# Kernel tuning notes

Measured on AMD Instinct MI355X. Metric: run time of the kernel, lower is better.

## Reference

```python
import jax, jax.numpy as jnp
import numpy as np

GROUPS = 32
EPS = 1e-5

def group_norm(x, w, b):
    # x: [B, C, T]
    B, C, T = x.shape
    g = x.reshape(B, GROUPS, C // GROUPS, T)
    mu = g.mean(axis=(2, 3), keepdims=True)
    var = g.var(axis=(2, 3), keepdims=True)
    g = (g - mu) * jax.lax.rsqrt(var + EPS)
    return g.reshape(B, C, T) * w[None, :, None] + b[None, :, None]

def conv1x1(x, w, b):
    # x: [B, C, T], w: [O, C], b: [O]
    return jnp.einsum('oc,bct->bot', w, x) + b[None, :, None]

def setup_inputs() -> dict:
    key = jax.random.key(0)
    ks = jax.random.split(key, 10)
    B, C, H, W = 128, 512, 16, 16
    d = {}
    d['criminal_cond'] = jax.random.normal(ks[0], (B, C, H, W), jnp.float32)
    d['morph_cond'] = jax.random.normal(ks[1], (B, C, H, W), jnp.float32)
    d['norm_w'] = jax.random.uniform(ks[2], (C,), jnp.float32, 0.5, 1.5)
    d['norm_b'] = 0.02 * jax.random.normal(ks[3], (C,), jnp.float32)
    d['qkv_w'] = jax.random.normal(ks[4], (3 * C, C), jnp.float32) / np.sqrt(C)
    d['qkv_b'] = 0.02 * jax.random.normal(ks[5], (3 * C,), jnp.float32)
    d['ekv_w'] = jax.random.normal(ks[6], (2 * C, C), jnp.float32) / np.sqrt(C)
    d['ekv_b'] = 0.02 * jax.random.normal(ks[7], (2 * C,), jnp.float32)
    d['proj_w'] = jax.random.normal(ks[8], (C, C), jnp.float32) / np.sqrt(C)
    d['proj_b'] = 0.02 * jax.random.normal(ks[9], (C,), jnp.float32)
    return d

def reference(criminal_cond, morph_cond, norm_w, norm_b, qkv_w, qkv_b, ekv_w, ekv_b, proj_w, proj_b):
    B, C, H, W = criminal_cond.shape
    x = criminal_cond.reshape(B, C, H * W)          # [B, C, T]
    cond = morph_cond.reshape(B, C, H * W)          # [B, C, S], S == T here
    h = group_norm(x, norm_w, norm_b)
    qkv = conv1x1(h, qkv_w, qkv_b)                  # [B, 3C, T]
    q, k, v = jnp.split(qkv, 3, axis=1)
    ekv = conv1x1(cond, ekv_w, ekv_b)               # [B, 2C, S]
    ek, ev = jnp.split(ekv, 2, axis=1)
    k = jnp.concatenate([ek, k], axis=-1)           # [B, C, S+T]
    v = jnp.concatenate([ev, v], axis=-1)
    scale = 1.0 / np.sqrt(np.sqrt(C))               # single head, head_dim = C
    logits = jnp.einsum('bct,bcs->bts', q * scale, k * scale)
    w = jax.nn.softmax(logits, axis=-1)             # [B, T, S+T]
    a = jnp.einsum('bts,bcs->bct', w, v)            # [B, C, T]
    hout = conv1x1(a, proj_w, proj_b)
    attn_out = (x + hout).reshape(B, C, H, W)
    return 2.0 * morph_cond - attn_out
```

## Files before the change

### kernel.cpp

```cpp
#include <hip/hip_runtime.h>
#include <hip/hip_bf16.h>
#include <math.h>

#define NB 128
#define NC 512
#define NT 256
#define NL 512
#define NG 32
#define SCALE2 0.04419417382415922f

typedef __attribute__((ext_vector_type(8))) short bf16x8;
typedef __attribute__((ext_vector_type(4))) float f32x4;
typedef __attribute__((ext_vector_type(4))) unsigned short u16x4;
typedef __attribute__((ext_vector_type(8))) unsigned short u16x8;
typedef __hip_bfloat16 bf16;

struct Params {
  const float *x, *morph, *qkvb, *ekvb, *projb;
  const bf16 *wq, *we, *wp;
  bf16 *hT, *mT, *qT, *kfT, *vf;
  float *out;
  int b0;
};

enum { M_QKV = 0, M_EKV = 1 };

__device__ inline unsigned short f2bf_bits(float f) {
  bf16 h = __float2bfloat16(f);
  return *reinterpret_cast<unsigned short*>(&h);
}

__device__ inline void gld16(const void* g, void* lds) {
  __builtin_amdgcn_global_load_lds(
      (const __attribute__((address_space(1))) unsigned int*)g,
      (__attribute__((address_space(3))) unsigned int*)lds, 16, 0, 0);
}

__global__ __launch_bounds__(256) void gn_stats_k(const float* __restrict__ x,
                                                  float* __restrict__ stats) {
  const int bg = blockIdx.x;
  const float4* p4 = (const float4*)(x + (size_t)bg * 4096);
  float s = 0.f, s2 = 0.f;
  #pragma unroll
  for (int i = 0; i < 4; ++i) {
    float4 v = p4[threadIdx.x + i * 256];
    s  += v.x + v.y + v.z + v.w;
    s2 += v.x * v.x + v.y * v.y + v.z * v.z + v.w * v.w;
  }
  #pragma unroll
  for (int off = 32; off; off >>= 1) {
    s  += __shfl_down(s, off);
    s2 += __shfl_down(s2, off);
  }
  __shared__ float red[8];
  const int wave = threadIdx.x >> 6, lane = threadIdx.x & 63;
  if (lane == 0) { red[wave * 2] = s; red[wave * 2 + 1] = s2; }
  __syncthreads();
  if (threadIdx.x == 0) {
    float S = 0.f, S2 = 0.f;
    for (int w = 0; w < 4; ++w) { S += red[w * 2]; S2 += red[w * 2 + 1]; }
    float mu = S * (1.0f / 4096.0f);
    float var = S2 * (1.0f / 4096.0f) - mu * mu;
    stats[bg * 2]     = mu;
    stats[bg * 2 + 1] = rsqrtf(var + 1e-5f);
  }
}

__global__ __launch_bounds__(256) void cvt_k(const float* __restrict__ s,
                                             bf16* __restrict__ d, int n) {
  int i = blockIdx.x * 256 + threadIdx.x;
  if (i < n) d[i] = __float2bfloat16(s[i]);
}

__global__ __launch_bounds__(256) void transpose2_k(const float* __restrict__ x,
                                                    const float* __restrict__ morph,
                                                    bf16* __restrict__ hT,
                                                    bf16* __restrict__ mT,
                                                    const float* __restrict__ stats,
                                                    const float* __restrict__ gnw,
                                                    const float* __restrict__ gnb,
                                                    int b0, int nbc) {
  __shared__ float sm[64][65];
  const int z = blockIdx.z;
  const int norm = (z < nbc) ? 1 : 0;
  const int lb = norm ? z : z - nbc;
  const int gb = b0 + lb;
  const float* src = norm ? x : morph;
  bf16* dst = norm ? hT : mT;
  const int t0 = blockIdx.x * 64, c0 = blockIdx.y * 64;
  const int tx = threadIdx.x & 15, ty = threadIdx.x >> 4;
  #pragma unroll
  for (int ci = 0; ci < 4; ++ci) {
    const int c = ty + ci * 16;
    const int cg = c0 + c;
    float4 v = *(const float4*)&src[((size_t)gb * NC + cg) * NT + t0 + tx * 4];
    if (norm) {
      float mu = stats[(gb * NG + (cg >> 4)) * 2];
      float rs = stats[(gb * NG + (cg >> 4)) * 2 + 1];
      float wv = gnw[cg], bv = gnb[cg];
      v.x = (v.x - mu) * rs * wv + bv;
      v.y = (v.y - mu) * rs * wv + bv;
      v.z = (v.z - mu) * rs * wv + bv;
      v.w = (v.w - mu) * rs * wv + bv;
    }
    sm[c][tx * 4 + 0] = v.x; sm[c][tx * 4 + 1] = v.y;
    sm[c][tx * 4 + 2] = v.z; sm[c][tx * 4 + 3] = v.w;
  }
  __syncthreads();
  const int t = threadIdx.x >> 2, cq = threadIdx.x & 3;
  u16x8 pk0, pk1;
  #pragma unroll
  for (int k = 0; k < 8; ++k) pk0[k] = f2bf_bits(sm[cq * 16 + k][t]);
  #pragma unroll
  for (int k = 0; k < 8; ++k) pk1[k] = f2bf_bits(sm[cq * 16 + 8 + k][t]);
  bf16* d = dst + ((size_t)lb * NT + t0 + t) * NC + c0 + cq * 16;
  *(u16x8*)d = pk0;
  *(u16x8*)(d + 8) = pk1;
}

template <int MODE>
__global__ __launch_bounds__(256) void gemm_k(Params P) {
  __shared__ unsigned short As[128][32];
  __shared__ unsigned short Bs[128][32];
  const int lb = blockIdx.x;
  const int m0 = blockIdx.y * 128;
  const int n0 = blockIdx.z * 128;
  const int tid = threadIdx.x;
  const int lane = tid & 63, w = tid >> 6;
  const int wr = w >> 1, wc = w & 1;
  const int ln = lane & 15, kq = lane >> 4;

  const bf16 *Ab, *Bb;
  if (MODE == M_QKV) { Ab = P.hT + (size_t)lb * NT * NC; Bb = P.wq; }
  else               { Ab = P.mT + (size_t)lb * NT * NC; Bb = P.we; }

  const char* Abase = (const char*)(Ab + (size_t)m0 * 512);
  const char* Bbase = (const char*)(Bb + (size_t)n0 * 512);

  const int r_lo = w * 32 + (lane >> 2);
  const int cid16 = (lane & 3) * 16;

  f32x4 acc[4][4] = {};

  for (int k0 = 0; k0 < 512; k0 += 32) {
    const size_t kb = (size_t)k0 * 2 + cid16;
    #pragma unroll
    for (int h = 0; h < 2; ++h) {
      const int rw = r_lo + h * 16;
      gld16(Abase + (size_t)rw * 1024 + kb, (char*)As + w * 2048 + h * 1024);
      gld16(Bbase + (size_t)rw * 1024 + kb, (char*)Bs + w * 2048 + h * 1024);
    }
    __syncthreads();
    bf16x8 af[4], bfr[4];
    #pragma unroll
    for (int i = 0; i < 4; ++i)
      af[i] = *(const bf16x8*)&As[wr * 64 + i * 16 + ln][kq * 8];
    #pragma unroll
    for (int j = 0; j < 4; ++j)
      bfr[j] = *(const bf16x8*)&Bs[wc * 64 + j * 16 + ln][kq * 8];
    #pragma unroll
    for (int i = 0; i < 4; ++i)
      #pragma unroll
      for (int j = 0; j < 4; ++j)
        acc[i][j] = __builtin_amdgcn_mfma_f32_16x16x32_bf16(af[i], bfr[j], acc[i][j], 0, 0, 0);
    __syncthreads();
  }

  #pragma unroll
  for (int i = 0; i < 4; ++i) {
    const int ig = m0 + wr * 64 + i * 16 + kq * 4;
    #pragma unroll
    for (int j = 0; j < 4; ++j) {
      const int jg = n0 + wc * 64 + j * 16 + ln;
      f32x4 a = acc[i][j];
      if (MODE == M_QKV) {
        float bias = P.qkvb[jg];
        if (jg < 512) {
          bf16* d = P.qT + ((size_t)lb * NT + ig) * NC + jg;
          #pragma unroll
          for (int r = 0; r < 4; ++r) d[(size_t)r * NC] = __float2bfloat16(a[r] + bias);
        } else if (jg < 1024) {
          bf16* d = P.kfT + ((size_t)lb * NL + 256 + ig) * NC + (jg - 512);
          #pragma unroll
          for (int r = 0; r < 4; ++r) d[(size_t)r * NC] = __float2bfloat16(a[r] + bias);
        } else {
          u16x4 pk;
          #pragma unroll
          for (int r = 0; r < 4; ++r) pk[r] = f2bf_bits(a[r] + bias);
          *(u16x4*)(P.vf + ((size_t)lb * NC + (jg - 1024)) * NL + 256 + ig) = pk;
        }
      } else {
        float bias = P.ekvb[jg];
        if (jg < 512) {
          bf16* d = P.kfT + ((size_t)lb * NL + ig) * NC + jg;
          #pragma unroll
          for (int r = 0; r < 4; ++r) d[(size_t)r * NC] = __float2bfloat16(a[r] + bias);
        } else {
          u16x4 pk;
          #pragma unroll
          for (int r = 0; r < 4; ++r) pk[r] = f2bf_bits(a[r] + bias);
          *(u16x4*)(P.vf + ((size_t)lb * NC + (jg - 512)) * NL + ig) = pk;
        }
      }
    }
  }
}

__global__ __launch_bounds__(256) void attn_k(Params P) {
  __shared__ unsigned short Abuf[32][32];
  __shared__ unsigned short Bbuf[512][32];
  __shared__ unsigned short Pbuf[32][520];
  __shared__ float redm[4][32];
  __shared__ float reds[4][32];

  const int lb = blockIdx.x, gb = P.b0 + lb;
  const int t0 = blockIdx.y * 32;
  const int tid = threadIdx.x;
  const int lane = tid & 63, w = tid >> 6;
  const int ln = lane & 15, kq = lane >> 4;
  const int srow = lane >> 2;
  const int scol = (lane & 3) * 16;

  const char* qg  = (const char*)(P.qT  + ((size_t)lb * NT + t0) * NC);
  const char* kg  = (const char*)(P.kfT + (size_t)lb * NL * NC);
  const char* vg  = (const char*)(P.vf  + (size_t)lb * NC * NL);
  const char* wpg = (const char*)P.wp;

  f32x4 sa[2][8] = {};
  bf16x8 af[2], bfr[8];

  for (int k0 = 0; k0 < 512; k0 += 32) {
    const size_t koff = (size_t)k0 * 2 + scol;
    if (w < 2)
      gld16(qg + (size_t)(w * 16 + srow) * 1024 + koff, (char*)Abuf + w * 1024);
    #pragma unroll
    for (int h = 0; h < 8; ++h)
      gld16(kg + (size_t)(w * 128 + h * 16 + srow) * 1024 + koff,
            (char*)Bbuf + w * 8192 + h * 1024);
    __syncthreads();
    af[0] = *(const bf16x8*)&Abuf[ln][kq * 8];
    af[1] = *(const bf16x8*)&Abuf[16 + ln][kq * 8];
    #pragma unroll
    for (int j = 0; j < 8; ++j)
      bfr[j] = *(const bf16x8*)&Bbuf[w * 128 + j * 16 + ln][kq * 8];
    #pragma unroll
    for (int i = 0; i < 2; ++i)
      #pragma unroll
      for (int j = 0; j < 8; ++j)
        sa[i][j] = __builtin_amdgcn_mfma_f32_16x16x32_bf16(af[i], bfr[j], sa[i][j], 0, 0, 0);
    __syncthreads();
  }

  float mx[2][4], sum[2][4], inv[2][4];
  #pragma unroll
  for (int i = 0; i < 2; ++i)
    #pragma unroll
    for (int r = 0; r < 4; ++r) {
      float m = -1e30f;
      #pragma unroll
      for (int j = 0; j < 8; ++j) m = fmaxf(m, sa[i][j][r]);
      mx[i][r] = m;
    }
  #pragma unroll
  for (int off = 1; off < 16; off <<= 1)
    #pragma unroll
    for (int i = 0; i < 2; ++i)
      #pragma unroll
      for (int r = 0; r < 4; ++r) mx[i][r] = fmaxf(mx[i][r], __shfl_xor(mx[i][r], off));
  if (ln == 0)
    #pragma unroll
    for (int i = 0; i < 2; ++i)
      #pragma unroll
      for (int r = 0; r < 4; ++r) redm[w][i * 16 + kq * 4 + r] = mx[i][r];
  __syncthreads();
  #pragma unroll
  for (int i = 0; i < 2; ++i)
    #pragma unroll
    for (int r = 0; r < 4; ++r) {
      const int row = i * 16 + kq * 4 + r;
      mx[i][r] = fmaxf(fmaxf(redm[0][row], redm[1][row]),
                       fmaxf(redm[2][row], redm[3][row]));
      sum[i][r] = 0.f;
    }
  #pragma unroll
  for (int i = 0; i < 2; ++i)
    #pragma unroll
    for (int j = 0; j < 8; ++j)
      #pragma unroll
      for (int r = 0; r < 4; ++r) {
        float e = __expf(SCALE2 * (sa[i][j][r] - mx[i][r]));
        sa[i][j][r] = e;
        sum[i][r] += e;
      }
  #pragma unroll
  for (int off = 1; off < 16; off <<= 1)
    #pragma unroll
    for (int i = 0; i < 2; ++i)
      #pragma unroll
      for (int r = 0; r < 4; ++r) sum[i][r] += __shfl_xor(sum[i][r], off);
  if (ln == 0)
    #pragma unroll
    for (int i = 0; i < 2; ++i)
      #pragma unroll
      for (int r = 0; r < 4; ++r) reds[w][i * 16 + kq * 4 + r] = sum[i][r];
  __syncthreads();
  #pragma unroll
  for (int i = 0; i < 2; ++i)
    #pragma unroll
    for (int r = 0; r < 4; ++r) {
      const int row = i * 16 + kq * 4 + r;
      inv[i][r] = 1.0f / (reds[0][row] + reds[1][row] + reds[2][row] + reds[3][row]);
    }
  #pragma unroll
  for (int i = 0; i < 2; ++i)
    #pragma unroll
    for (int j = 0; j < 8; ++j)
      #pragma unroll
      for (int r = 0; r < 4; ++r)
        Pbuf[i * 16 + kq * 4 + r][w * 128 + j * 16 + ln] = f2bf_bits(sa[i][j][r] * inv[i][r]);
  __syncthreads();

  f32x4 oa[2][8] = {};
  for (int k0 = 0; k0 < 512; k0 += 32) {
    const size_t koff = (size_t)k0 * 2 + scol;
    #pragma unroll
    for (int h = 0; h < 8; ++h)
      gld16(vg + (size_t)(w * 128 + h * 16 + srow) * 1024 + koff,
            (char*)Bbuf + w * 8192 + h * 1024);
    __syncthreads();
    af[0] = *(const bf16x8*)&Pbuf[ln][k0 + kq * 8];
    af[1] = *(const bf16x8*)&Pbuf[16 + ln][k0 + kq * 8];
    #pragma unroll
    for (int j = 0; j < 8; ++j)
      bfr[j] = *(const bf16x8*)&Bbuf[w * 128 + j * 16 + ln][kq * 8];
    #pragma unroll
    for (int i = 0; i < 2; ++i)
      #pragma unroll
      for (int j = 0; j < 8; ++j)
        oa[i][j] = __builtin_amdgcn_mfma_f32_16x16x32_bf16(af[i], bfr[j], oa[i][j], 0, 0, 0);
    __syncthreads();
  }

  #pragma unroll
  for (int i = 0; i < 2; ++i)
    #pragma unroll
    for (int j = 0; j < 8; ++j)
      #pragma unroll
      for (int r = 0; r < 4; ++r)
        Pbuf[i * 16 + kq * 4 + r][w * 128 + j * 16 + ln] = f2bf_bits(oa[i][j][r]);
  __syncthreads();

  f32x4 za[2][8] = {};
  for (int k0 = 0; k0 < 512; k0 += 32) {
    const size_t koff = (size_t)k0 * 2 + scol;
    #pragma unroll
    for (int h = 0; h < 8; ++h)
      gld16(wpg + (size_t)(w * 128 + h * 16 + srow) * 1024 + koff,
            (char*)Bbuf + w * 8192 + h * 1024);
    __syncthreads();
    af[0] = *(const bf16x8*)&Pbuf[ln][k0 + kq * 8];
    af[1] = *(const bf16x8*)&Pbuf[16 + ln][k0 + kq * 8];
    #pragma unroll
    for (int j = 0; j < 8; ++j)
      bfr[j] = *(const bf16x8*)&Bbuf[w * 128 + j * 16 + ln][kq * 8];
    #pragma unroll
    for (int i = 0; i < 2; ++i)
      #pragma unroll
      for (int j = 0; j < 8; ++j)
        za[i][j] = __builtin_amdgcn_mfma_f32_16x16x32_bf16(af[i], bfr[j], za[i][j], 0, 0, 0);
    __syncthreads();
  }

  #pragma unroll
  for (int i = 0; i < 2; ++i) {
    const int trow = t0 + i * 16 + kq * 4;
    #pragma unroll
    for (int j = 0; j < 8; ++j) {
      const int c = w * 128 + j * 16 + ln;
      const float bias = P.projb[c];
      const size_t idx = ((size_t)gb * NC + c) * NT + trow;
      float4 mo = *(const float4*)&P.morph[idx];
      float4 xx = *(const float4*)&P.x[idx];
      f32x4 o;
      o[0] = 2.0f * mo.x - xx.x - (za[i][j][0] + bias);
      o[1] = 2.0f * mo.y - xx.y - (za[i][j][1] + bias);
      o[2] = 2.0f * mo.z - xx.z - (za[i][j][2] + bias);
      o[3] = 2.0f * mo.w - xx.w - (za[i][j][3] + bias);
      *(f32x4*)&P.out[idx] = o;
    }
  }
}

extern "C" void kernel_launch(void* const* d_in, const int* in_sizes, int n_in,
                              void* d_out, int out_size, void* d_ws, size_t ws_size,
                              hipStream_t stream) {
  const float* x     = (const float*)d_in[0];
  const float* morph = (const float*)d_in[1];
  const float* gnw   = (const float*)d_in[2];
  const float* gnb   = (const float*)d_in[3];
  const float* qkvw  = (const float*)d_in[4];
  const float* qkvb  = (const float*)d_in[5];
  const float* ekvw  = (const float*)d_in[6];
  const float* ekvb  = (const float*)d_in[7];
  const float* projw = (const float*)d_in[8];
  const float* projb = (const float*)d_in[9];

  bf16* wq = (bf16*)d_ws;
  bf16* we = wq + 786432;
  bf16* wp = we + 524288;
  float* stats = (float*)(wp + 262144);
  bf16* pb = (bf16*)(stats + 8192);

  const size_t per_b = 917504;
  const size_t fixed = (size_t)(786432 + 524288 + 262144) * 2 + 8192 * 4;
  int nbc = NB;
  while (nbc > 1 && fixed + (size_t)nbc * per_b * 2 > ws_size) nbc >>= 1;

  Params P;
  P.x = x; P.morph = morph; P.qkvb = qkvb; P.ekvb = ekvb; P.projb = projb;
  P.wq = wq; P.we = we; P.wp = wp;
  P.hT  = pb;  pb += (size_t)nbc * 131072;
  P.mT  = pb;  pb += (size_t)nbc * 131072;
  P.qT  = pb;  pb += (size_t)nbc * 131072;
  P.kfT = pb;  pb += (size_t)nbc * 262144;
  P.vf  = pb;
  P.out = (float*)d_out;

  gn_stats_k<<<dim3(NB * NG), dim3(256), 0, stream>>>(x, stats);
  cvt_k<<<dim3(3072), dim3(256), 0, stream>>>(qkvw, wq, 786432);
  cvt_k<<<dim3(2048), dim3(256), 0, stream>>>(ekvw, we, 524288);
  cvt_k<<<dim3(1024), dim3(256), 0, stream>>>(projw, wp, 262144);

  for (int b0 = 0; b0 < NB; b0 += nbc) {
    P.b0 = b0;
    transpose2_k<<<dim3(4, 8, 2 * nbc), dim3(256), 0, stream>>>(
        x, morph, P.hT, P.mT, stats, gnw, gnb, b0, nbc);
    gemm_k<M_QKV><<<dim3(nbc, 2, 12), dim3(256), 0, stream>>>(P);
    gemm_k<M_EKV><<<dim3(nbc, 2, 8),  dim3(256), 0, stream>>>(P);
    attn_k       <<<dim3(nbc, 8),     dim3(256), 0, stream>>>(P);
  }
}
```

Baseline: 539.2 us.

## Load attention MFMA operands directly from global memory, dropping LDS staging

The three GEMM phases in the attention kernel (QK^T, PV, output projection) now read their B operands, and for QK^T also the A operand, straight from global memory into registers. The shared-memory staging buffers and the per-iteration barriers are removed. This cuts LDS traffic and synchronisation and frees shared memory for occupancy. In exchange, each wave issues strided 16-byte global loads with no cross-wave reuse, relying on the L1/L2 caches for the K/V/Wp tiles that every block rereads.

```diff
diff --git a/kernel.cpp b/kernel.cpp
--- a/kernel.cpp
+++ b/kernel.cpp
@@ -207,8 +207,6 @@
 }
 
 __global__ __launch_bounds__(256) void attn_k(Params P) {
-  __shared__ unsigned short Abuf[32][32];
-  __shared__ unsigned short Bbuf[512][32];
   __shared__ unsigned short Pbuf[32][520];
   __shared__ float redm[4][32];
   __shared__ float reds[4][32];
@@ -218,37 +216,30 @@
   const int tid = threadIdx.x;
   const int lane = tid & 63, w = tid >> 6;
   const int ln = lane & 15, kq = lane >> 4;
-  const int srow = lane >> 2;
-  const int scol = (lane & 3) * 16;
-
-  const char* qg  = (const char*)(P.qT  + ((size_t)lb * NT + t0) * NC);
-  const char* kg  = (const char*)(P.kfT + (size_t)lb * NL * NC);
-  const char* vg  = (const char*)(P.vf  + (size_t)lb * NC * NL);
-  const char* wpg = (const char*)P.wp;
+
+  const bf16* qg  = P.qT  + ((size_t)lb * NT + t0) * NC;
+  const bf16* kg  = P.kfT + (size_t)lb * NL * NC;
+  const bf16* vg  = P.vf  + (size_t)lb * NC * NL;
+  const bf16* wpg = P.wp;
 
   f32x4 sa[2][8] = {};
   bf16x8 af[2], bfr[8];
 
-  for (int k0 = 0; k0 < 512; k0 += 32) {
-    const size_t koff = (size_t)k0 * 2 + scol;
-    if (w < 2)
-      gld16(qg + (size_t)(w * 16 + srow) * 1024 + koff, (char*)Abuf + w * 1024);
-    #pragma unroll
-    for (int h = 0; h < 8; ++h)
-      gld16(kg + (size_t)(w * 128 + h * 16 + srow) * 1024 + koff,
-            (char*)Bbuf + w * 8192 + h * 1024);
-    __syncthreads();
-    af[0] = *(const bf16x8*)&Abuf[ln][kq * 8];
-    af[1] = *(const bf16x8*)&Abuf[16 + ln][kq * 8];
-    #pragma unroll
-    for (int j = 0; j < 8; ++j)
-      bfr[j] = *(const bf16x8*)&Bbuf[w * 128 + j * 16 + ln][kq * 8];
-    #pragma unroll
-    for (int i = 0; i < 2; ++i)
+  {
+    const bf16* qa0 = qg + (size_t)ln * NC + kq * 8;
+    const bf16* kb0 = kg + (size_t)(w * 128 + ln) * NC + kq * 8;
+    for (int k0 = 0; k0 < 512; k0 += 32) {
+      af[0] = *(const bf16x8*)(qa0 + k0);
+      af[1] = *(const bf16x8*)(qa0 + (size_t)16 * NC + k0);
       #pragma unroll
       for (int j = 0; j < 8; ++j)
-        sa[i][j] = __builtin_amdgcn_mfma_f32_16x16x32_bf16(af[i], bfr[j], sa[i][j], 0, 0, 0);
-    __syncthreads();
+        bfr[j] = *(const bf16x8*)(kb0 + (size_t)j * 16 * NC + k0);
+      #pragma unroll
+      for (int i = 0; i < 2; ++i)
+        #pragma unroll
+        for (int j = 0; j < 8; ++j)
+          sa[i][j] = __builtin_amdgcn_mfma_f32_16x16x32_bf16(af[i], bfr[j], sa[i][j], 0, 0, 0);
+    }
   }
 
   float mx[2][4], sum[2][4], inv[2][4];
@@ -321,25 +312,22 @@
   __syncthreads();
 
   f32x4 oa[2][8] = {};
-  for (int k0 = 0; k0 < 512; k0 += 32) {
-    const size_t koff = (size_t)k0 * 2 + scol;
-    #pragma unroll
-    for (int h = 0; h < 8; ++h)
-      gld16(vg + (size_t)(w * 128 + h * 16 + srow) * 1024 + koff,
-            (char*)Bbuf + w * 8192 + h * 1024);
-    __syncthreads();
-    af[0] = *(const bf16x8*)&Pbuf[ln][k0 + kq * 8];
-    af[1] = *(const bf16x8*)&Pbuf[16 + ln][k0 + kq * 8];
-    #pragma unroll
-    for (int j = 0; j < 8; ++j)
-      bfr[j] = *(const bf16x8*)&Bbuf[w * 128 + j * 16 + ln][kq * 8];
-    #pragma unroll
-    for (int i = 0; i < 2; ++i)
+  {
+    const bf16* vb0 = vg + (size_t)(w * 128 + ln) * NL + kq * 8;
+    for (int k0 = 0; k0 < 512; k0 += 32) {
+      af[0] = *(const bf16x8*)&Pbuf[ln][k0 + kq * 8];
+      af[1] = *(const bf16x8*)&Pbuf[16 + ln][k0 + kq * 8];
       #pragma unroll
       for (int j = 0; j < 8; ++j)
-        oa[i][j] = __builtin_amdgcn_mfma_f32_16x16x32_bf16(af[i], bfr[j], oa[i][j], 0, 0, 0);
-    __syncthreads();
-  }
+        bfr[j] = *(const bf16x8*)(vb0 + (size_t)j * 16 * NL + k0);
+      #pragma unroll
+      for (int i = 0; i < 2; ++i)
+        #pragma unroll
+        for (int j = 0; j < 8; ++j)
+          oa[i][j] = __builtin_amdgcn_mfma_f32_16x16x32_bf16(af[i], bfr[j], oa[i][j], 0, 0, 0);
+    }
+  }
+  __syncthreads();
 
   #pragma unroll
   for (int i = 0; i < 2; ++i)
@@ -351,24 +339,20 @@
   __syncthreads();
 
   f32x4 za[2][8] = {};
-  for (int k0 = 0; k0 < 512; k0 += 32) {
-    const size_t koff = (size_t)k0 * 2 + scol;
-    #pragma unroll
-    for (int h = 0; h < 8; ++h)
-      gld16(wpg + (size_t)(w * 128 + h * 16 + srow) * 1024 + koff,
-            (char*)Bbuf + w * 8192 + h * 1024);
-    __syncthreads();
-    af[0] = *(const bf16x8*)&Pbuf[ln][k0 + kq * 8];
-    af[1] = *(const bf16x8*)&Pbuf[16 + ln][k0 + kq * 8];
-    #pragma unroll
-    for (int j = 0; j < 8; ++j)
-      bfr[j] = *(const bf16x8*)&Bbuf[w * 128 + j * 16 + ln][kq * 8];
-    #pragma unroll
-    for (int i = 0; i < 2; ++i)
+  {
+    const bf16* wb0 = wpg + (size_t)(w * 128 + ln) * NC + kq * 8;
+    for (int k0 = 0; k0 < 512; k0 += 32) {
+      af[0] = *(const bf16x8*)&Pbuf[ln][k0 + kq * 8];
+      af[1] = *(const bf16x8*)&Pbuf[16 + ln][k0 + kq * 8];
       #pragma unroll
       for (int j = 0; j < 8; ++j)
-        za[i][j] = __builtin_amdgcn_mfma_f32_16x16x32_bf16(af[i], bfr[j], za[i][j], 0, 0, 0);
-    __syncthreads();
+        bfr[j] = *(const bf16x8*)(wb0 + (size_t)j * 16 * NC + k0);
+      #pragma unroll
+      for (int i = 0; i < 2; ++i)
+        #pragma unroll
+        for (int j = 0; j < 8; ++j)
+          za[i][j] = __builtin_amdgcn_mfma_f32_16x16x32_bf16(af[i], bfr[j], za[i][j], 0, 0, 0);
+    }
   }
 
   #pragma unroll
```

Measured after the change: 602.2 us. +11.7%, slower.

## Split fused attention kernel into softmax plus tiled PV and projection GEMMs

Applied to the files above, without the earlier changes.

Merges the QKV and EKV input GEMMs into a single launch, selecting the mode from the block z index. The monolithic attention kernel, which handled 32 query rows per block through QK, softmax, PV and the projection, is split into three kernels. A softmax kernel writes probabilities to global memory, reusing the q buffer. Two 128x128-tiled GEMM kernels then compute P·V (stored into the k buffer) and the output projection with the residual epilogue. The aim is better operand reuse and more parallelism in the PV and projection stages, at the cost of extra global round-trips and launches.

```diff
diff --git a/kernel.cpp b/kernel.cpp
--- a/kernel.cpp
+++ b/kernel.cpp
@@ -22,8 +22,6 @@
   float *out;
   int b0;
 };
-
-enum { M_QKV = 0, M_EKV = 1 };
 
 __device__ inline unsigned short f2bf_bits(float f) {
   bf16 h = __float2bfloat16(f);
@@ -118,21 +116,21 @@
   *(u16x8*)(d + 8) = pk1;
 }
 
-template <int MODE>
-__global__ __launch_bounds__(256) void gemm_k(Params P) {
+__global__ __launch_bounds__(256) void gemm_in_k(Params P) {
   __shared__ unsigned short As[128][32];
   __shared__ unsigned short Bs[128][32];
   const int lb = blockIdx.x;
   const int m0 = blockIdx.y * 128;
-  const int n0 = blockIdx.z * 128;
+  const int z = blockIdx.z;
+  const bool qkv = (z < 12);
+  const int n0 = (qkv ? z : z - 12) * 128;
   const int tid = threadIdx.x;
   const int lane = tid & 63, w = tid >> 6;
   const int wr = w >> 1, wc = w & 1;
   const int ln = lane & 15, kq = lane >> 4;
 
-  const bf16 *Ab, *Bb;
-  if (MODE == M_QKV) { Ab = P.hT + (size_t)lb * NT * NC; Bb = P.wq; }
-  else               { Ab = P.mT + (size_t)lb * NT * NC; Bb = P.we; }
+  const bf16* Ab = (qkv ? P.hT : P.mT) + (size_t)lb * NT * NC;
+  const bf16* Bb = qkv ? P.wq : P.we;
 
   const char* Abase = (const char*)(Ab + (size_t)m0 * 512);
   const char* Bbase = (const char*)(Bb + (size_t)n0 * 512);
@@ -173,7 +171,7 @@
     for (int j = 0; j < 4; ++j) {
       const int jg = n0 + wc * 64 + j * 16 + ln;
       f32x4 a = acc[i][j];
-      if (MODE == M_QKV) {
+      if (qkv) {
         float bias = P.qkvb[jg];
         if (jg < 512) {
           bf16* d = P.qT + ((size_t)lb * NT + ig) * NC + jg;
@@ -206,14 +204,13 @@
   }
 }
 
-__global__ __launch_bounds__(256) void attn_k(Params P) {
+__global__ __launch_bounds__(256) void att_sm_k(Params P) {
   __shared__ unsigned short Abuf[32][32];
   __shared__ unsigned short Bbuf[512][32];
-  __shared__ unsigned short Pbuf[32][520];
   __shared__ float redm[4][32];
   __shared__ float reds[4][32];
 
-  const int lb = blockIdx.x, gb = P.b0 + lb;
+  const int lb = blockIdx.x;
   const int t0 = blockIdx.y * 32;
   const int tid = threadIdx.x;
   const int lane = tid & 63, w = tid >> 6;
@@ -221,10 +218,8 @@
   const int srow = lane >> 2;
   const int scol = (lane & 3) * 16;
 
-  const char* qg  = (const char*)(P.qT  + ((size_t)lb * NT + t0) * NC);
-  const char* kg  = (const char*)(P.kfT + (size_t)lb * NL * NC);
-  const char* vg  = (const char*)(P.vf  + (size_t)lb * NC * NL);
-  const char* wpg = (const char*)P.wp;
+  const char* qg = (const char*)(P.qT  + ((size_t)lb * NT + t0) * NC);
+  const char* kg = (const char*)(P.kfT + (size_t)lb * NL * NC);
 
   f32x4 sa[2][8] = {};
   bf16x8 af[2], bfr[8];
@@ -311,82 +306,92 @@
       const int row = i * 16 + kq * 4 + r;
       inv[i][r] = 1.0f / (reds[0][row] + reds[1][row] + reds[2][row] + reds[3][row]);
     }
+
+  bf16* pdst = P.qT + ((size_t)lb * NT + t0) * NL;
   #pragma unroll
   for (int i = 0; i < 2; ++i)
     #pragma unroll
     for (int j = 0; j < 8; ++j)
       #pragma unroll
       for (int r = 0; r < 4; ++r)
-        Pbuf[i * 16 + kq * 4 + r][w * 128 + j * 16 + ln] = f2bf_bits(sa[i][j][r] * inv[i][r]);
-  __syncthreads();
-
-  f32x4 oa[2][8] = {};
+        pdst[(size_t)(i * 16 + kq * 4 + r) * NL + w * 128 + j * 16 + ln] =
+            __float2bfloat16(sa[i][j][r] * inv[i][r]);
+}
+
+template <int MODE>
+__global__ __launch_bounds__(256) void gemm_att(Params P) {
+  __shared__ unsigned short As[128][32];
+  __shared__ unsigned short Bs[128][32];
+  const int lb = blockIdx.x;
+  const int m0 = blockIdx.y * 128;
+  const int n0 = blockIdx.z * 128;
+  const int tid = threadIdx.x;
+  const int lane = tid & 63, w = tid >> 6;
+  const int wr = w >> 1, wc = w & 1;
+  const int ln = lane & 15, kq = lane >> 4;
+
+  const bf16 *Ab, *Bb;
+  if (MODE == 1) { Ab = P.qT  + (size_t)lb * 131072; Bb = P.vf + (size_t)lb * NC * NL; }
+  else           { Ab = P.kfT + (size_t)lb * 262144; Bb = P.wp; }
+
+  const char* Abase = (const char*)(Ab + (size_t)m0 * 512);
+  const char* Bbase = (const char*)(Bb + (size_t)n0 * 512);
+
+  const int r_lo = w * 32 + (lane >> 2);
+  const int cid16 = (lane & 3) * 16;
+
+  f32x4 acc[4][4] = {};
+
   for (int k0 = 0; k0 < 512; k0 += 32) {
-    const size_t koff = (size_t)k0 * 2 + scol;
-    #pragma unroll
-    for (int h = 0; h < 8; ++h)
-      gld16(vg + (size_t)(w * 128 + h * 16 + srow) * 1024 + koff,
-            (char*)Bbuf + w * 8192 + h * 1024);
-    __syncthreads();
-    af[0] = *(const bf16x8*)&Pbuf[ln][k0 + kq * 8];
-    af[1] = *(const bf16x8*)&Pbuf[16 + ln][k0 + kq * 8];
-    #pragma unroll
-    for (int j = 0; j < 8; ++j)
-      bfr[j] = *(const bf16x8*)&Bbuf[w * 128 + j * 16 + ln][kq * 8];
-    #pragma unroll
-    for (int i = 0; i < 2; ++i)
-      #pragma unroll
-      for (int j = 0; j < 8; ++j)
-        oa[i][j] = __builtin_amdgcn_mfma_f32_16x16x32_bf16(af[i], bfr[j], oa[i][j], 0, 0, 0);
-    __syncthreads();
-  }
-
-  #pragma unroll
-  for (int i = 0; i < 2; ++i)
-    #pragma unroll
-    for (int j = 0; j < 8; ++j)
-      #pragma unroll
-      for (int r = 0; r < 4; ++r)
-        Pbuf[i * 16 + kq * 4 + r][w * 128 + j * 16 + ln] = f2bf_bits(oa[i][j][r]);
-  __syncthreads();
-
-  f32x4 za[2][8] = {};
-  for (int k0 = 0; k0 < 512; k0 += 32) {
-    const size_t koff = (size_t)k0 * 2 + scol;
-    #pragma unroll
-    for (int h = 0; h < 8; ++h)
-      gld16(wpg + (size_t)(w * 128 + h * 16 + srow) * 1024 + koff,
-            (char*)Bbuf + w * 8192 + h * 1024);
-    __syncthreads();
-    af[0] = *(const bf16x8*)&Pbuf[ln][k0 + kq * 8];
-    af[1] = *(const bf16x8*)&Pbuf[16 + ln][k0 + kq * 8];
-    #pragma unroll
-    for (int j = 0; j < 8; ++j)
-      bfr[j] = *(const bf16x8*)&Bbuf[w * 128 + j * 16 + ln][kq * 8];
-    #pragma unroll
-    for (int i = 0; i < 2; ++i)
-      #pragma unroll
-      for (int j = 0; j < 8; ++j)
-        za[i][j] = __builtin_amdgcn_mfma_f32_16x16x32_bf16(af[i], bfr[j], za[i][j], 0, 0, 0);
-    __syncthreads();
-  }
-
-  #pragma unroll
-  for (int i = 0; i < 2; ++i) {
-    const int trow = t0 + i * 16 + kq * 4;
-    #pragma unroll
-    for (int j = 0; j < 8; ++j) {
-      const int c = w * 128 + j * 16 + ln;
-      const float bias = P.projb[c];
-      const size_t idx = ((size_t)gb * NC + c) * NT + trow;
-      float4 mo = *(const float4*)&P.morph[idx];
-      float4 xx = *(const float4*)&P.x[idx];
-      f32x4 o;
-      o[0] = 2.0f * mo.x - xx.x - (za[i][j][0] + bias);
-      o[1] = 2.0f * mo.y - xx.y - (za[i][j][1] + bias);
-      o[2] = 2.0f * mo.z - xx.z - (za[i][j][2] + bias);
-      o[3] = 2.0f * mo.w - xx.w - (za[i][j][3] + bias);
-      *(f32x4*)&P.out[idx] = o;
+    const size_t kb = (size_t)k0 * 2 + cid16;
+    #pragma unroll
+    for (int h = 0; h < 2; ++h) {
+      const int rw = r_lo + h * 16;
+      gld16(Abase + (size_t)rw * 1024 + kb, (char*)As + w * 2048 + h * 1024);
+      gld16(Bbase + (size_t)rw * 1024 + kb, (char*)Bs + w * 2048 + h * 1024);
+    }
+    __syncthreads();
+    bf16x8 af[4], bfr[4];
+    #pragma unroll
+    for (int i = 0; i < 4; ++i)
+      af[i] = *(const bf16x8*)&As[wr * 64 + i * 16 + ln][kq * 8];
+    #pragma unroll
+    for (int j = 0; j < 4; ++j)
+      bfr[j] = *(const bf16x8*)&Bs[wc * 64 + j * 16 + ln][kq * 8];
+    #pragma unroll
+    for (int i = 0; i < 4; ++i)
+      #pragma unroll
+      for (int j = 0; j < 4; ++j)
+        acc[i][j] = __builtin_amdgcn_mfma_f32_16x16x32_bf16(af[i], bfr[j], acc[i][j], 0, 0, 0);
+    __syncthreads();
+  }
+
+  bf16* Og = P.kfT + (size_t)lb * 262144;
+  const int gb = P.b0 + lb;
+
+  #pragma unroll
+  for (int i = 0; i < 4; ++i) {
+    const int ig = m0 + wr * 64 + i * 16 + kq * 4;
+    #pragma unroll
+    for (int j = 0; j < 4; ++j) {
+      const int jg = n0 + wc * 64 + j * 16 + ln;
+      f32x4 a = acc[i][j];
+      if (MODE == 1) {
+        bf16* d = Og + (size_t)ig * NC + jg;
+        #pragma unroll
+        for (int r = 0; r < 4; ++r) d[(size_t)r * NC] = __float2bfloat16(a[r]);
+      } else {
+        const float bias = P.projb[jg];
+        const size_t idx = ((size_t)gb * NC + jg) * NT + ig;
+        float4 mo = *(const float4*)&P.morph[idx];
+        float4 xx = *(const float4*)&P.x[idx];
+        f32x4 o;
+        o[0] = 2.0f * mo.x - xx.x - (a[0] + bias);
+        o[1] = 2.0f * mo.y - xx.y - (a[1] + bias);
+        o[2] = 2.0f * mo.z - xx.z - (a[2] + bias);
+        o[3] = 2.0f * mo.w - xx.w - (a[3] + bias);
+        *(f32x4*)&P.out[idx] = o;
+      }
     }
   }
 }
@@ -435,8 +440,9 @@
     P.b0 = b0;
     transpose2_k<<<dim3(4, 8, 2 * nbc), dim3(256), 0, stream>>>(
         x, morph, P.hT, P.mT, stats, gnw, gnb, b0, nbc);
-    gemm_k<M_QKV><<<dim3(nbc, 2, 12), dim3(256), 0, stream>>>(P);
-    gemm_k<M_EKV><<<dim3(nbc, 2, 8),  dim3(256), 0, stream>>>(P);
-    attn_k       <<<dim3(nbc, 8),     dim3(256), 0, stream>>>(P);
-  }
-}
+    gemm_in_k  <<<dim3(nbc, 2, 20), dim3(256), 0, stream>>>(P);
+    att_sm_k   <<<dim3(nbc, 8),     dim3(256), 0, stream>>>(P);
+    gemm_att<1><<<dim3(nbc, 2, 4),  dim3(256), 0, stream>>>(P);
+    gemm_att<2><<<dim3(nbc, 2, 4),  dim3(256), 0, stream>>>(P);
+  }
+}
```

Measured after the change: 537.0 us. Within noise of the previous version (-0.4%).
